# Optimization experiments

Hardware: AMD Instinct MI355X
Metric: run time of the kernel (lower is better)

## Reference

```python
import jax, jax.numpy as jnp
import numpy as np

H = 1024      # hidden_size
V = 32000     # vocab_size
MAX_LEN = 32  # decode steps
B = 64        # batch


def _uni(key, shape, s):
    return jax.random.uniform(key, shape, jnp.float32, -s, s)


def setup_inputs() -> dict:
    key = jax.random.key(0)
    ks = jax.random.split(key, 10)
    s = 1.0 / np.sqrt(H)
    return {
        "vectors": jax.random.normal(ks[0], (B, H), jnp.float32),
        "W_fc_in": _uni(ks[1], (H, H), s),
        "b_fc_in": _uni(ks[2], (H,), s),
        "W_ih": _uni(ks[3], (3 * H, H), s),   # torch GRU weight_ih_l0 (r,z,n)
        "W_hh": _uni(ks[4], (3 * H, H), s),
        "b_ih": _uni(ks[5], (3 * H,), s),
        "b_hh": _uni(ks[6], (3 * H,), s),
        "W_out": _uni(ks[7], (V, H), s),
        "b_out": _uni(ks[8], (V,), s),
        "top_k": 8,
    }


def reference(vectors, W_fc_in, b_fc_in, W_ih, W_hh, b_ih, b_hh, W_out, b_out, top_k):
    # hidden = fc_in(vectors); initial GRU input is zeros
    h0 = vectors @ W_fc_in.T + b_fc_in           # [B, H]
    x0 = jnp.zeros_like(h0)

    def gru_cell(carry, _):
        h, x = carry
        gi = x @ W_ih.T + b_ih                   # [B, 3H]
        gh = h @ W_hh.T + b_hh                   # [B, 3H]
        i_r, i_z, i_n = jnp.split(gi, 3, axis=-1)
        h_r, h_z, h_n = jnp.split(gh, 3, axis=-1)
        r = jax.nn.sigmoid(i_r + h_r)
        z = jax.nn.sigmoid(i_z + h_z)
        n = jnp.tanh(i_n + r * h_n)
        h_new = (1.0 - z) * n + z * h            # PyTorch GRU update
        # out == h_new for single-layer GRU; inputs = out feeds back
        return (h_new, h_new), h_new

    _, outs = jax.lax.scan(gru_cell, (h0, x0), None, length=MAX_LEN)  # [T, B, H]

    # fc_out + log_softmax over vocab, for all steps at once
    logits = jnp.einsum('tbh,vh->tbv', outs, W_out) + b_out           # [T, B, V]
    logp = jax.nn.log_softmax(logits, axis=-1)

    # topk then multinomial over exp(top logp) == categorical over top logp
    top_p, top_i = jax.lax.top_k(logp, top_k)                         # [T, B, K]
    samp = jax.random.categorical(jax.random.key(42), top_p, axis=-1)  # [T, B]
    tokens = jnp.take_along_axis(top_i, samp[..., None], axis=-1)[..., 0]
    return tokens.T.astype(jnp.int32)                                  # [B, T]
```

## Files before the change

kernel.cpp:

```cpp
#include <hip/hip_runtime.h>
#include <stdint.h>

typedef unsigned int u32;
typedef unsigned long long u64;
typedef unsigned short ushort;
typedef __attribute__((ext_vector_type(8))) short bf16x8;
typedef __attribute__((ext_vector_type(4))) float f32x4;

#define JAX_PARTITIONABLE 1

#define HD     1024
#define BBATCH 64
#define TSTEP  32
#define VOCAB  32000
#define NROWS  2048
#define GATE6  6144
#define NCB    250
#define NCAND  16

__device__ __forceinline__ void threefry2x32(u32 k0, u32 k1, u32 x0, u32 x1,
                                             u32& y0, u32& y1) {
  u32 ks2 = k0 ^ k1 ^ 0x1BD11BDAu;
  x0 += k0; x1 += k1;
#define TFR(r) do { x0 += x1; x1 = (x1 << (r)) | (x1 >> (32 - (r))); x1 ^= x0; } while (0)
  TFR(13); TFR(15); TFR(26); TFR(6);   x0 += k1;  x1 += ks2 + 1u;
  TFR(17); TFR(29); TFR(16); TFR(24);  x0 += ks2; x1 += k0 + 2u;
  TFR(13); TFR(15); TFR(26); TFR(6);   x0 += k0;  x1 += k1 + 3u;
  TFR(17); TFR(29); TFR(16); TFR(24);  x0 += k1;  x1 += ks2 + 4u;
  TFR(13); TFR(15); TFR(26); TFR(6);   x0 += ks2; x1 += k0 + 5u;
#undef TFR
  y0 = x0; y1 = x1;
}

__device__ __forceinline__ u32 jax_random_bits(u32 n) {
#if JAX_PARTITIONABLE
  u32 y0, y1; threefry2x32(0u, 42u, 0u, n, y0, y1);
  return y0 ^ y1;
#else
  u32 y0, y1;
  if (n < 8192u) { threefry2x32(0u, 42u, n, n + 8192u, y0, y1); return y0; }
  else           { threefry2x32(0u, 42u, n - 8192u, n, y0, y1); return y1; }
#endif
}

__device__ __forceinline__ u64 packkey(float v, int idx) {
  u32 b = __float_as_uint(v);
  b = (b & 0x80000000u) ? ~b : (b | 0x80000000u);
  return ((u64)b << 32) | (u64)(~(u32)idx);
}

__device__ __forceinline__ void insert4(u64* t4, u64 k) {
  if (k > t4[3]) {
    t4[3] = k;
    if (t4[3] > t4[2]) { u64 tm = t4[2]; t4[2] = t4[3]; t4[3] = tm; }
    if (t4[2] > t4[1]) { u64 tm = t4[1]; t4[1] = t4[2]; t4[2] = tm; }
    if (t4[1] > t4[0]) { u64 tm = t4[0]; t4[0] = t4[1]; t4[1] = tm; }
  }
}

__device__ __forceinline__ ushort f2bf_rne(float x) {
  u32 u = __float_as_uint(x);
  return (ushort)((u + 0x7fffu + ((u >> 16) & 1u)) >> 16);
}
__device__ __forceinline__ float bf2f(ushort h) {
  return __uint_as_float(((u32)h) << 16);
}

typedef const __attribute__((address_space(1))) void* gas_ptr;
typedef __attribute__((address_space(3))) void* las_ptr;
__device__ __forceinline__ void gload16(const void* g, void* l) {
  __builtin_amdgcn_global_load_lds((gas_ptr)g, (las_ptr)l, 16, 0, 0);
}

__global__ __launch_bounds__(256) void tobf16(const float* __restrict__ src,
                                              ushort* __restrict__ dst, int n8) {
  int i = blockIdx.x * 256 + threadIdx.x;
  const int stride = gridDim.x * 256;
  for (; i < n8; i += stride) {
    const float4* s4 = (const float4*)src + (size_t)i * 2;
    float4 a = s4[0], b = s4[1];
    u32 o0 = f2bf_rne(a.x) | ((u32)f2bf_rne(a.y) << 16);
    u32 o1 = f2bf_rne(a.z) | ((u32)f2bf_rne(a.w) << 16);
    u32 o2 = f2bf_rne(b.x) | ((u32)f2bf_rne(b.y) << 16);
    u32 o3 = f2bf_rne(b.z) | ((u32)f2bf_rne(b.w) << 16);
    ((uint4*)dst)[i] = make_uint4(o0, o1, o2, o3);
  }
}

__global__ __launch_bounds__(256) void tobf16x3_gruP(
    const float* __restrict__ Wih, const float* __restrict__ Whh,
    ushort* __restrict__ w1, ushort* __restrict__ w2, ushort* __restrict__ w3) {
  int i = blockIdx.x * 256 + threadIdx.x;
  if (i >= GATE6 * (HD / 8)) return;
  int rp = i >> 7;
  int kc = i & 127;
  int b = rp / 48, rem = rp % 48;
  int g = rem >> 3, jp = rem & 7;
  const float* src = (g < 3)
      ? (Wih + ((size_t)g * HD + b * 8 + jp) * HD)
      : (Whh + ((size_t)(g - 3) * HD + b * 8 + jp) * HD);
  const float4* s4 = (const float4*)(src + kc * 8);
  float v[8];
  float4 a = s4[0], bb = s4[1];
  v[0]=a.x; v[1]=a.y; v[2]=a.z; v[3]=a.w; v[4]=bb.x; v[5]=bb.y; v[6]=bb.z; v[7]=bb.w;
  ushort p1[8], p2[8], p3[8];
#pragma unroll
  for (int e = 0; e < 8; ++e) {
    p1[e] = f2bf_rne(v[e]);
    float r1 = v[e] - bf2f(p1[e]);
    p2[e] = f2bf_rne(r1);
    float r2 = r1 - bf2f(p2[e]);
    p3[e] = f2bf_rne(r2);
  }
  u32 o1[4], o2[4], o3[4];
#pragma unroll
  for (int e = 0; e < 4; ++e) {
    o1[e] = p1[2*e] | ((u32)p1[2*e+1] << 16);
    o2[e] = p2[2*e] | ((u32)p2[2*e+1] << 16);
    o3[e] = p3[2*e] | ((u32)p3[2*e+1] << 16);
  }
  ((uint4*)w1)[i] = make_uint4(o1[0], o1[1], o1[2], o1[3]);
  ((uint4*)w2)[i] = make_uint4(o2[0], o2[1], o2[2], o2[3]);
  ((uint4*)w3)[i] = make_uint4(o3[0], o3[1], o3[2], o3[3]);
}

__global__ __launch_bounds__(256) void gemm64_nt(
    const float* __restrict__ A, const float* __restrict__ B,
    float* __restrict__ part) {
  __shared__ float4 As4[64 * 33];
  __shared__ float4 Bs4[32 * 33];
  const int tid = threadIdx.x;
  const int n0 = blockIdx.x * 32;
  const float* Brow = B + (size_t)n0 * HD;
  const int ks = blockIdx.y * 256;
  const int tc = tid & 7, trg = tid >> 3;
  float acc[2][4] = {};
  for (int kc = 0; kc < 2; ++kc) {
    const int k0 = ks + kc * 128;
#pragma unroll
    for (int l = 0; l < 8; ++l) {
      int m = tid + l * 256; int row = m >> 5, k4 = m & 31;
      As4[row * 33 + k4] = *(const float4*)(A + (size_t)row * HD + k0 + k4 * 4);
    }
#pragma unroll
    for (int l = 0; l < 4; ++l) {
      int m = tid + l * 256; int row = m >> 5, k4 = m & 31;
      Bs4[row * 33 + k4] = *(const float4*)(Brow + (size_t)row * HD + k0 + k4 * 4);
    }
    __syncthreads();
#pragma unroll
    for (int kq = 0; kq < 32; ++kq) {
      float4 av[2], bv[4];
      av[0] = As4[trg * 33 + kq];
      av[1] = As4[(trg + 32) * 33 + kq];
      bv[0] = Bs4[tc * 33 + kq];
      bv[1] = Bs4[(tc + 8) * 33 + kq];
      bv[2] = Bs4[(tc + 16) * 33 + kq];
      bv[3] = Bs4[(tc + 24) * 33 + kq];
#pragma unroll
      for (int i = 0; i < 2; ++i)
#pragma unroll
        for (int j = 0; j < 4; ++j) {
          acc[i][j] += av[i].x * bv[j].x;
          acc[i][j] += av[i].y * bv[j].y;
          acc[i][j] += av[i].z * bv[j].z;
          acc[i][j] += av[i].w * bv[j].w;
        }
    }
    __syncthreads();
  }
  float* P = part + (size_t)blockIdx.y * BBATCH * HD;
#pragma unroll
  for (int i = 0; i < 2; ++i) {
    int b = trg + 32 * i;
#pragma unroll
    for (int j = 0; j < 4; ++j)
      P[(size_t)b * HD + n0 + tc + 8 * j] = acc[i][j];
  }
}

__global__ __launch_bounds__(256) void combine_fcin(
    const float* __restrict__ part, const float* __restrict__ b_fc,
    float* __restrict__ h, ushort* __restrict__ h1, ushort* __restrict__ h2,
    ushort* __restrict__ h3) {
  int idx = blockIdx.x * 256 + threadIdx.x;
  int j = idx & 1023; int b = idx >> 10;
  const size_t S = (size_t)BBATCH * HD;
  const float* p = part + (size_t)b * HD;
  float d = p[j]; d += p[S + j]; d += p[2 * S + j]; d += p[3 * S + j];
  float hv = d + b_fc[j];
  h[idx] = hv;
  ushort a = f2bf_rne(hv);
  float r1 = hv - bf2f(a);
  ushort bb = f2bf_rne(r1);
  float r2 = r1 - bf2f(bb);
  h1[idx] = a; h2[idx] = bb; h3[idx] = f2bf_rne(r2);
}

__global__ __launch_bounds__(128) void gru_step(
    const ushort* __restrict__ W1, const ushort* __restrict__ W2,
    const ushort* __restrict__ W3,
    const float* __restrict__ b_ih, const float* __restrict__ b_hh,
    float* __restrict__ h, float* __restrict__ outs,
    ushort* __restrict__ outs_bf,
    ushort* __restrict__ h1, ushort* __restrict__ h2, ushort* __restrict__ h3,
    int t) {
  __shared__ ushort Bs[2][3][3072];
  const int tid = threadIdx.x;
  const int lane = tid & 63, w = tid >> 6;
  const int b = blockIdx.x >> 1;
  const int hb = blockIdx.x & 1;
  const ushort* B1g = W1 + (size_t)b * 48 * HD;
  const ushort* B2g = W2 + (size_t)b * 48 * HD;
  const ushort* B3g = W3 + (size_t)b * 48 * HD;
  const int rc = lane >> 3;
  const int gr8 = ((lane & 7) ^ rc) * 8;
  const int l15 = lane & 15;
  const int kc4 = lane >> 4;
  const int arow = hb * 32 + w * 16 + l15;

#define STAGE_B(buf, kt) do {                                         \
    const int k0_ = (kt) * 64;                                        \
    _Pragma("unroll")                                                 \
    for (int c_ = 0; c_ < 9; ++c_) {                                  \
      int q_ = w * 9 + c_;                                            \
      const ushort* src_; ushort* dst_;                               \
      if (q_ < 6)       { src_ = B1g + (size_t)(q_ * 8 + rc) * HD;    \
                          dst_ = &Bs[buf][0][q_ * 512]; }             \
      else if (q_ < 12) { src_ = B2g + (size_t)((q_ - 6) * 8 + rc) * HD; \
                          dst_ = &Bs[buf][1][(q_ - 6) * 512]; }       \
      else              { src_ = B3g + (size_t)((q_ - 12) * 8 + rc) * HD; \
                          dst_ = &Bs[buf][2][(q_ - 12) * 512]; }      \
      gload16(src_ + k0_ + gr8, dst_);                                \
    }                                                                 \
  } while (0)

#define LOAD_A(dst, kt) do {                                          \
    _Pragma("unroll")                                                 \
    for (int ks_ = 0; ks_ < 2; ++ks_) {                               \
      const int ke_ = (kt) * 64 + ks_ * 32 + kc4 * 8;                 \
      dst[ks_][0] = *(const bf16x8*)(h1 + (size_t)arow * HD + ke_);   \
      dst[ks_][1] = *(const bf16x8*)(h2 + (size_t)arow * HD + ke_);   \
      dst[ks_][2] = *(const bf16x8*)(h3 + (size_t)arow * HD + ke_);   \
    }                                                                 \
  } while (0)

#define COMPUTE_G(AR, buf) do {                                       \
    _Pragma("unroll")                                                 \
    for (int ks_ = 0; ks_ < 2; ++ks_) {                               \
      const int kb_ = ks_ * 64 + kc4 * 16;                            \
      bf16x8 b1_[3], b2_[3], b3_[3];                                  \
      _Pragma("unroll")                                               \
      for (int nt_ = 0; nt_ < 3; ++nt_) {                             \
        int br_ = nt_ * 16 + l15;                                     \
        int bo_ = br_ * 128 + (kb_ ^ ((br_ & 7) << 4));               \
        b1_[nt_] = *(const bf16x8*)((const char*)&Bs[buf][0][0] + bo_); \
        b2_[nt_] = *(const bf16x8*)((const char*)&Bs[buf][1][0] + bo_); \
        b3_[nt_] = *(const bf16x8*)((const char*)&Bs[buf][2][0] + bo_); \
      }                                                               \
      _Pragma("unroll")                                               \
      for (int nt_ = 0; nt_ < 3; ++nt_) {                             \
        acc[nt_] = __builtin_amdgcn_mfma_f32_16x16x32_bf16(AR[ks_][2], b1_[nt_], acc[nt_], 0, 0, 0); \
        acc[nt_] = __builtin_amdgcn_mfma_f32_16x16x32_bf16(AR[ks_][0], b3_[nt_], acc[nt_], 0, 0, 0); \
        acc[nt_] = __builtin_amdgcn_mfma_f32_16x16x32_bf16(AR[ks_][1], b2_[nt_], acc[nt_], 0, 0, 0); \
        acc[nt_] = __builtin_amdgcn_mfma_f32_16x16x32_bf16(AR[ks_][1], b1_[nt_], acc[nt_], 0, 0, 0); \
        acc[nt_] = __builtin_amdgcn_mfma_f32_16x16x32_bf16(AR[ks_][0], b2_[nt_], acc[nt_], 0, 0, 0); \
        acc[nt_] = __builtin_amdgcn_mfma_f32_16x16x32_bf16(AR[ks_][0], b1_[nt_], acc[nt_], 0, 0, 0); \
      }                                                               \
    }                                                                 \
  } while (0)

  f32x4 acc[3];
#pragma unroll
  for (int nt = 0; nt < 3; ++nt) acc[nt] = (f32x4){0.f, 0.f, 0.f, 0.f};

  bf16x8 aA[2][3], aB[2][3];
  LOAD_A(aA, 0); STAGE_B(0, 0);
  LOAD_A(aB, 1); STAGE_B(1, 1);

#pragma unroll
  for (int kt2 = 0; kt2 < 8; ++kt2) {
    const int kte = kt2 * 2, kto = kte + 1;
    asm volatile("s_waitcnt vmcnt(15)" ::: "memory");
    __builtin_amdgcn_s_barrier();
    __builtin_amdgcn_sched_barrier(0);
    COMPUTE_G(aA, 0);
    __builtin_amdgcn_sched_barrier(0);
    __builtin_amdgcn_s_barrier();
    if (kte + 2 < 16) { LOAD_A(aA, kte + 2); STAGE_B(0, kte + 2); }
    if (kto < 15) {
      asm volatile("s_waitcnt vmcnt(15)" ::: "memory");
    } else {
      asm volatile("s_waitcnt vmcnt(0)" ::: "memory");
    }
    __builtin_amdgcn_s_barrier();
    __builtin_amdgcn_sched_barrier(0);
    COMPUTE_G(aB, 1);
    __builtin_amdgcn_sched_barrier(0);
    __builtin_amdgcn_s_barrier();
    if (kto + 2 < 16) { LOAD_A(aB, kto + 2); STAGE_B(1, kto + 2); }
  }
#undef STAGE_B
#undef LOAD_A
#undef COMPUTE_G

  const bool low = (l15 < 8);
  const int j = b * 8 + l15;
  float bi_r = 0.f, bi_z = 0.f, bi_n = 0.f, bh_r = 0.f, bh_z = 0.f, bh_n = 0.f;
  if (low) {
    bi_r = b_ih[j]; bi_z = b_ih[HD + j]; bi_n = b_ih[2 * HD + j];
    bh_r = b_hh[j]; bh_z = b_hh[HD + j]; bh_n = b_hh[2 * HD + j];
  }
#pragma unroll
  for (int r = 0; r < 4; ++r) {
    float v0 = acc[0][r], v1 = acc[1][r], v2 = acc[2][r];
    float p0 = __shfl_xor(v0, 8);
    float p1 = __shfl_xor(v1, 8);
    float p2 = __shfl_xor(v2, 8);
    if (low) {
      float gir = (t == 0) ? bi_r : (v0 + bi_r);
      float giz = (t == 0) ? bi_z : (p0 + bi_z);
      float gin = (t == 0) ? bi_n : (v1 + bi_n);
      float ghr = p1 + bh_r;
      float ghz = v2 + bh_z;
      float ghn = p2 + bh_n;
      float rr = 1.0f / (1.0f + expf(-(gir + ghr)));
      float zz = 1.0f / (1.0f + expf(-(giz + ghz)));
      float nn = tanhf(gin + rr * ghn);
      int i = hb * 32 + w * 16 + (lane >> 4) * 4 + r;
      int idx = i * HD + j;
      float hp = h[idx];
      float hn2 = (1.0f - zz) * nn + zz * hp;
      h[idx] = hn2;
      size_t o = ((size_t)t * BBATCH + i) * HD + j;
      outs[o] = hn2;
      ushort a = f2bf_rne(hn2);
      outs_bf[o] = a;
      float r1 = hn2 - bf2f(a);
      ushort bb2 = f2bf_rne(r1);
      float r2 = r1 - bf2f(bb2);
      h1[idx] = a; h2[idx] = bb2; h3[idx] = f2bf_rne(r2);
    }
  }
}

__global__ __launch_bounds__(256) void gemm_out_mfma(
    const ushort* __restrict__ Abf, const ushort* __restrict__ Bbf,
    const float* __restrict__ b_out, u64* __restrict__ keys) {
  __shared__ ushort Sm[4][4096];
  __shared__ float Cs[32 * 133];
  u64* pkL1 = (u64*)&Sm[0][0];
  u64* pkL2 = pkL1 + 1024;

  const int tid = threadIdx.x;
  const int lane = tid & 63;
  const int wid = tid >> 6;
  const int wr = wid >> 1, wc = wid & 1;
  const int cb = blockIdx.y;
  const int n0 = cb * 128;
  const int r0 = blockIdx.x * 128;

  const ushort* Ag = Abf + (size_t)r0 * HD;
  const ushort* Bg = Bbf + (size_t)n0 * HD;
  const int rc4 = lane >> 2;
  const int gs8 = ((lane & 3) ^ ((lane >> 3) & 3)) * 8;
  const int l15 = lane & 15;
  const int swoff = (((lane >> 4) ^ ((l15 >> 1) & 3)) << 4);

#define STAGE_OUT(AB, BB, k0) do {                                   \
    _Pragma("unroll")                                                \
    for (int c_ = 0; c_ < 2; ++c_) {                                 \
      int ch_ = wid * 2 + c_;                                        \
      int row_ = ch_ * 16 + rc4;                                     \
      gload16(Ag + (size_t)row_ * HD + (k0) + gs8, (AB) + ch_ * 512);\
      gload16(Bg + (size_t)row_ * HD + (k0) + gs8, (BB) + ch_ * 512);\
    }                                                                \
  } while (0)

#define COMPUTE_OUT(AB, BB) do {                                     \
    bf16x8 a_[4], b_[4];                                             \
    _Pragma("unroll")                                                \
    for (int m_ = 0; m_ < 4; ++m_)                                   \
      a_[m_] = *(const bf16x8*)((const char*)(AB) +                  \
               (wr * 64 + m_ * 16 + l15) * 64 + swoff);              \
    _Pragma("unroll")                                                \
    for (int n_ = 0; n_ < 4; ++n_)                                   \
      b_[n_] = *(const bf16x8*)((const char*)(BB) +                  \
               (wc * 64 + n_ * 16 + l15) * 64 + swoff);              \
    _Pragma("unroll")                                                \
    for (int m_ = 0; m_ < 4; ++m_)                                   \
      _Pragma("unroll")                                              \
      for (int n_ = 0; n_ < 4; ++n_)                                 \
        acc[m_][n_] = __builtin_amdgcn_mfma_f32_16x16x32_bf16(       \
            a_[m_], b_[n_], acc[m_][n_], 0, 0, 0);                   \
  } while (0)

  float bo[4];
#pragma unroll
  for (int n = 0; n < 4; ++n) bo[n] = b_out[n0 + wc * 64 + n * 16 + l15];

  f32x4 acc[4][4];
#pragma unroll
  for (int m = 0; m < 4; ++m)
#pragma unroll
    for (int n = 0; n < 4; ++n) acc[m][n] = (f32x4){0.f, 0.f, 0.f, 0.f};

  STAGE_OUT(Sm[0], Sm[2], 0);
  int p = 0;
  for (int kp = 0; kp < 32; ++kp) {
    if (kp < 31) {
      STAGE_OUT(Sm[p ^ 1], Sm[2 + (p ^ 1)], (kp + 1) * 32);
      asm volatile("s_waitcnt vmcnt(4)" ::: "memory");
    } else {
      asm volatile("s_waitcnt vmcnt(0)" ::: "memory");
    }
    __builtin_amdgcn_s_barrier();
    __builtin_amdgcn_sched_barrier(0);
    COMPUTE_OUT(Sm[p], Sm[2 + p]);
    __builtin_amdgcn_sched_barrier(0);
    __builtin_amdgcn_s_barrier();
    p ^= 1;
  }

#pragma unroll
  for (int q = 0; q < 4; ++q) {
    if (wr == (q >> 1)) {
#pragma unroll
      for (int mi = 0; mi < 2; ++mi) {
        const int m = (q & 1) * 2 + mi;
#pragma unroll
        for (int n = 0; n < 4; ++n) {
          int c = wc * 64 + n * 16 + l15;
#pragma unroll
          for (int j = 0; j < 4; ++j) {
            int lr = mi * 16 + (lane >> 4) * 4 + j;
            Cs[lr * 133 + c] = acc[m][n][j] + bo[n];
          }
        }
      }
    }
    __syncthreads();
    {
      int rr = tid >> 3, seg = tid & 7;
      const float* rp = Cs + rr * 133 + seg * 16;
      u64 t4[4] = {0, 0, 0, 0};
#pragma unroll
      for (int c = 0; c < 16; ++c) insert4(t4, packkey(rp[c], n0 + seg * 16 + c));
      u64* d = pkL1 + (rr * 8 + seg) * 4;
      d[0] = t4[0]; d[1] = t4[1]; d[2] = t4[2]; d[3] = t4[3];
    }
    __syncthreads();
    if (tid < 64) {
      int rr = tid >> 1, hf = tid & 1;
      const u64* s = pkL1 + (rr * 8 + hf * 4) * 4;
      u64 t4[4] = {s[0], s[1], s[2], s[3]};
#pragma unroll
      for (int e = 4; e < 16; ++e) insert4(t4, s[e]);
      u64* d = pkL2 + tid * 4;
      d[0] = t4[0]; d[1] = t4[1]; d[2] = t4[2]; d[3] = t4[3];
    }
    __syncthreads();
    if (tid < 32) {
      const u64* s = pkL2 + tid * 8;
      u64 t4[4] = {s[0], s[1], s[2], s[3]};
      insert4(t4, s[4]); insert4(t4, s[5]); insert4(t4, s[6]); insert4(t4, s[7]);
      int grow = r0 + q * 32 + tid;
      u64* kp2 = keys + ((size_t)grow * NCB + cb) * 4;
      kp2[0] = t4[0]; kp2[1] = t4[1]; kp2[2] = t4[2]; kp2[3] = t4[3];
    }
    __syncthreads();
  }
#undef STAGE_OUT
#undef COMPUTE_OUT
}

__global__ __launch_bounds__(64) void merge_sample2(
    const u64* __restrict__ keys, const float* __restrict__ outs,
    const float* __restrict__ W_out, const float* __restrict__ b_out,
    int* __restrict__ out) {
  const int r = blockIdx.x;
  const int lane = threadIdx.x;
  __shared__ float row_f[1024];
  {
    const float4* src = (const float4*)(outs + (size_t)r * HD);
    float4* dst = (float4*)row_f;
#pragma unroll
    for (int m = 0; m < 4; ++m) dst[lane + m * 64] = src[lane + m * 64];
  }
  u64 t8[8] = {0, 0, 0, 0, 0, 0, 0, 0};
  const u64* KR = keys + (size_t)r * 1000;
#pragma unroll
  for (int m = 0; m < 16; ++m) {
    int i = lane + (m << 6);
    if (i < 1000) {
      u64 k = KR[i];
      if (k > t8[7]) {
        t8[7] = k;
#pragma unroll
        for (int e = 7; e > 0; --e) {
          u64 hi = t8[e - 1], lo = t8[e];
          t8[e - 1] = (lo > hi) ? lo : hi;
          t8[e]     = (lo > hi) ? hi : lo;
        }
      }
    }
  }
  const int mycand = lane >> 2;
  u64 myw = 0;
#pragma unroll
  for (int it = 0; it < NCAND; ++it) {
    u64 bmax = t8[0];
#pragma unroll
    for (int o = 32; o; o >>= 1) {
      u64 x = __shfl_xor(bmax, o);
      if (x > bmax) bmax = x;
    }
    if (it == mycand) myw = bmax;
    if (t8[0] == bmax) {
#pragma unroll
      for (int e = 0; e < 7; ++e) t8[e] = t8[e + 1];
      t8[7] = 0;
    }
  }
  const int myvi = (int)(~(u32)(myw & 0xffffffffu));
  float mysum;
  {
    const float4* wrow = (const float4*)(W_out + (size_t)myvi * HD);
    const float4* rf = (const float4*)row_f;
    const int q = lane & 3;
    float s = 0.f;
#pragma unroll
    for (int m2 = 0; m2 < 64; ++m2) {
      float4 a = rf[q + m2 * 4];
      float4 bb = wrow[q + m2 * 4];
      s += a.x * bb.x; s += a.y * bb.y; s += a.z * bb.z; s += a.w * bb.w;
    }
    s += __shfl_xor(s, 1);
    s += __shfl_xor(s, 2);
    mysum = s + b_out[myvi];
  }
  float v[NCAND]; int vi[NCAND];
#pragma unroll
  for (int c = 0; c < NCAND; ++c) {
    v[c] = __shfl(mysum, c * 4);
    vi[c] = __shfl(myvi, c * 4);
  }
  if (lane == 0) {
#pragma unroll
    for (int a = 0; a < 8; ++a)
#pragma unroll
      for (int b2 = a + 1; b2 < NCAND; ++b2) {
        bool sw = (v[b2] > v[a]) || (v[b2] == v[a] && vi[b2] < vi[a]);
        if (sw) {
          float tf = v[a]; v[a] = v[b2]; v[b2] = tf;
          int ti = vi[a]; vi[a] = vi[b2]; vi[b2] = ti;
        }
      }
    const float M = v[0];
    const float TINY = 1.17549435e-38f;
    float best = -3.4e38f; int bi = 0;
#pragma unroll
    for (int k = 0; k < 8; ++k) {
      float lp = v[k] - M;
      u32 bits = jax_random_bits((u32)(r * 8 + k));
      float f = __uint_as_float((bits >> 9) | 0x3f800000u) - 1.0f;
      float u = f * (1.0f - TINY) + TINY;
      u = fmaxf(TINY, u);
      float g = -logf(-logf(u));
      float s = g + lp;
      if (s > best) { best = s; bi = k; }
    }
    int t = r >> 6, b = r & 63;
    out[b * TSTEP + t] = vi[bi];
  }
}

extern "C" void kernel_launch(void* const* d_in, const int* in_sizes, int n_in,
                              void* d_out, int out_size, void* d_ws, size_t ws_size,
                              hipStream_t stream) {
  (void)in_sizes; (void)n_in; (void)out_size; (void)ws_size;
  const float* vectors = (const float*)d_in[0];
  const float* W_fc_in = (const float*)d_in[1];
  const float* b_fc_in = (const float*)d_in[2];
  const float* W_ih    = (const float*)d_in[3];
  const float* W_hh    = (const float*)d_in[4];
  const float* b_ih    = (const float*)d_in[5];
  const float* b_hh    = (const float*)d_in[6];
  const float* W_out   = (const float*)d_in[7];
  const float* b_out   = (const float*)d_in[8];
  int* out = (int*)d_out;

  char* w = (char*)d_ws;
  float* h = (float*)w;          w += (size_t)BBATCH * HD * 4;
  float* outs = (float*)w;       w += (size_t)NROWS * HD * 4;
  ushort* outs_bf = (ushort*)w;  w += (size_t)NROWS * HD * 2;
  ushort* Wbf = (ushort*)w;      w += (size_t)VOCAB * HD * 2;
  char* X = w;                   w += (size_t)3 * GATE6 * HD * 2;
  ushort* Wg1 = (ushort*)X;
  ushort* Wg2 = Wg1 + (size_t)GATE6 * HD;
  ushort* Wg3 = Wg2 + (size_t)GATE6 * HD;
  u64* keys = (u64*)X;
  ushort* h1 = (ushort*)w;       w += (size_t)BBATCH * HD * 2;
  ushort* h2 = (ushort*)w;       w += (size_t)BBATCH * HD * 2;
  ushort* h3 = (ushort*)w;       w += (size_t)BBATCH * HD * 2;
  float* part = (float*)w;

  tobf16<<<4096, 256, 0, stream>>>(W_out, Wbf, VOCAB * HD / 8);
  tobf16x3_gruP<<<GATE6 * (HD / 8) / 256, 256, 0, stream>>>(W_ih, W_hh,
                                                            Wg1, Wg2, Wg3);

  gemm64_nt<<<dim3(32, 4), 256, 0, stream>>>(vectors, W_fc_in, part);
  combine_fcin<<<256, 256, 0, stream>>>(part, b_fc_in, h, h1, h2, h3);

  for (int t = 0; t < TSTEP; ++t)
    gru_step<<<256, 128, 0, stream>>>(Wg1, Wg2, Wg3, b_ih, b_hh,
                                      h, outs, outs_bf, h1, h2, h3, t);

  gemm_out_mfma<<<dim3(16, NCB), 256, 0, stream>>>(outs_bf, Wbf, b_out, keys);

  merge_sample2<<<NROWS, 64, 0, stream>>>(keys, outs, W_out, b_out, out);
}
```

Baseline: 1.166 ms.

## Double K-tile depth in output GEMM and regroup GRU block mapping

```diff
diff --git a/kernel.cpp b/kernel.cpp
--- a/kernel.cpp
+++ b/kernel.cpp
@@ -208,8 +208,10 @@
   __shared__ ushort Bs[2][3][3072];
   const int tid = threadIdx.x;
   const int lane = tid & 63, w = tid >> 6;
-  const int b = blockIdx.x >> 1;
-  const int hb = blockIdx.x & 1;
+  const int grp = blockIdx.x >> 4;
+  const int rmd = blockIdx.x & 15;
+  const int hb = rmd >> 3;
+  const int b = grp * 8 + (rmd & 7);
   const ushort* B1g = W1 + (size_t)b * 48 * HD;
   const ushort* B2g = W2 + (size_t)b * 48 * HD;
   const ushort* B3g = W3 + (size_t)b * 48 * HD;
@@ -347,9 +349,9 @@
 __global__ __launch_bounds__(256) void gemm_out_mfma(
     const ushort* __restrict__ Abf, const ushort* __restrict__ Bbf,
     const float* __restrict__ b_out, u64* __restrict__ keys) {
-  __shared__ ushort Sm[4][4096];
-  __shared__ float Cs[32 * 133];
-  u64* pkL1 = (u64*)&Sm[0][0];
+  __shared__ ushort Sm[2][2][8192];
+  float* Cs = (float*)&Sm[0][0][0];
+  u64* pkL1 = (u64*)((char*)&Sm[0][0][0] + 17024);
   u64* pkL2 = pkL1 + 1024;
 
   const int tid = threadIdx.x;
@@ -362,37 +364,50 @@
 
   const ushort* Ag = Abf + (size_t)r0 * HD;
   const ushort* Bg = Bbf + (size_t)n0 * HD;
-  const int rc4 = lane >> 2;
-  const int gs8 = ((lane & 3) ^ ((lane >> 3) & 3)) * 8;
+  const int rc = lane >> 3;
+  const int gr8 = ((lane & 7) ^ rc) * 8;
   const int l15 = lane & 15;
-  const int swoff = (((lane >> 4) ^ ((l15 >> 1) & 3)) << 4);
-
-#define STAGE_OUT(AB, BB, k0) do {                                   \
+  const int kseg = (lane >> 4) * 16;
+
+#define STAGE_OUT(buf, kt) do {                                      \
+    ushort* SA_ = &Sm[buf][0][0];                                    \
+    ushort* SB_ = &Sm[buf][1][0];                                    \
+    const int k0_ = (kt) * 64;                                       \
     _Pragma("unroll")                                                \
-    for (int c_ = 0; c_ < 2; ++c_) {                                 \
-      int ch_ = wid * 2 + c_;                                        \
-      int row_ = ch_ * 16 + rc4;                                     \
-      gload16(Ag + (size_t)row_ * HD + (k0) + gs8, (AB) + ch_ * 512);\
-      gload16(Bg + (size_t)row_ * HD + (k0) + gs8, (BB) + ch_ * 512);\
+    for (int c_ = 0; c_ < 4; ++c_) {                                 \
+      int ch_ = wid * 4 + c_;                                        \
+      int row_ = ch_ * 8 + rc;                                       \
+      gload16(Ag + (size_t)row_ * HD + k0_ + gr8, SA_ + ch_ * 512);  \
+      gload16(Bg + (size_t)row_ * HD + k0_ + gr8, SB_ + ch_ * 512);  \
     }                                                                \
   } while (0)
 
-#define COMPUTE_OUT(AB, BB) do {                                     \
-    bf16x8 a_[4], b_[4];                                             \
+#define COMPUTE_OUT(buf) do {                                        \
+    const ushort* SA_ = &Sm[buf][0][0];                              \
+    const ushort* SB_ = &Sm[buf][1][0];                              \
     _Pragma("unroll")                                                \
-    for (int m_ = 0; m_ < 4; ++m_)                                   \
-      a_[m_] = *(const bf16x8*)((const char*)(AB) +                  \
-               (wr * 64 + m_ * 16 + l15) * 64 + swoff);              \
-    _Pragma("unroll")                                                \
-    for (int n_ = 0; n_ < 4; ++n_)                                   \
-      b_[n_] = *(const bf16x8*)((const char*)(BB) +                  \
-               (wc * 64 + n_ * 16 + l15) * 64 + swoff);              \
-    _Pragma("unroll")                                                \
-    for (int m_ = 0; m_ < 4; ++m_)                                   \
+    for (int ks_ = 0; ks_ < 2; ++ks_) {                              \
+      bf16x8 a_[4], b_[4];                                           \
+      const int kb_ = ks_ * 64 + kseg;                               \
       _Pragma("unroll")                                              \
-      for (int n_ = 0; n_ < 4; ++n_)                                 \
-        acc[m_][n_] = __builtin_amdgcn_mfma_f32_16x16x32_bf16(       \
-            a_[m_], b_[n_], acc[m_][n_], 0, 0, 0);                   \
+      for (int m_ = 0; m_ < 4; ++m_) {                               \
+        int row_ = wr * 64 + m_ * 16 + l15;                          \
+        int off_ = row_ * 128 + (kb_ ^ ((row_ & 7) << 4));           \
+        a_[m_] = *(const bf16x8*)((const char*)SA_ + off_);          \
+      }                                                              \
+      _Pragma("unroll")                                              \
+      for (int n_ = 0; n_ < 4; ++n_) {                               \
+        int row_ = wc * 64 + n_ * 16 + l15;                          \
+        int off_ = row_ * 128 + (kb_ ^ ((row_ & 7) << 4));           \
+        b_[n_] = *(const bf16x8*)((const char*)SB_ + off_);          \
+      }                                                              \
+      _Pragma("unroll")                                              \
+      for (int m_ = 0; m_ < 4; ++m_)                                 \
+        _Pragma("unroll")                                            \
+        for (int n_ = 0; n_ < 4; ++n_)                               \
+          acc[m_][n_] = __builtin_amdgcn_mfma_f32_16x16x32_bf16(     \
+              a_[m_], b_[n_], acc[m_][n_], 0, 0, 0);                 \
+    }                                                                \
   } while (0)
 
   float bo[4];
@@ -405,22 +420,23 @@
 #pragma unroll
     for (int n = 0; n < 4; ++n) acc[m][n] = (f32x4){0.f, 0.f, 0.f, 0.f};
 
-  STAGE_OUT(Sm[0], Sm[2], 0);
+  STAGE_OUT(0, 0);
   int p = 0;
-  for (int kp = 0; kp < 32; ++kp) {
-    if (kp < 31) {
-      STAGE_OUT(Sm[p ^ 1], Sm[2 + (p ^ 1)], (kp + 1) * 32);
-      asm volatile("s_waitcnt vmcnt(4)" ::: "memory");
+  for (int kt = 0; kt < 16; ++kt) {
+    if (kt < 15) {
+      STAGE_OUT(p ^ 1, kt + 1);
+      asm volatile("s_waitcnt vmcnt(8)" ::: "memory");
     } else {
       asm volatile("s_waitcnt vmcnt(0)" ::: "memory");
     }
     __builtin_amdgcn_s_barrier();
     __builtin_amdgcn_sched_barrier(0);
-    COMPUTE_OUT(Sm[p], Sm[2 + p]);
+    COMPUTE_OUT(p);
     __builtin_amdgcn_sched_barrier(0);
     __builtin_amdgcn_s_barrier();
     p ^= 1;
   }
+  __syncthreads();
 
 #pragma unroll
   for (int q = 0; q < 4; ++q) {
```

Result: faster. 1.070 ms (-8.2%).
